# Kernel optimization log

Hardware: AMD Instinct MI355X
Metric: run time of the kernel (lower is better)

The kernel has to match this reference:

```python
import jax, jax.numpy as jnp
import numpy as np

nT, nB, H, V = 256, 256, 1024, 32000

def setup_inputs() -> dict:
    key = jax.random.key(0)
    ks = jax.random.split(key, 16)
    s = 0.02
    return {
        "tokens": jax.random.randint(ks[0], (nB,), 0, V),
        "prev_hidden": jax.random.normal(ks[1], (1, nB, H), dtype=jnp.float32),
        "enc_outputs": jax.random.normal(ks[2], (nT, nB, H), dtype=jnp.float32),
        "emb": jax.random.normal(ks[3], (V, H), dtype=jnp.float32) * s,
        "W_i2h": jax.random.normal(ks[4], (H, H), dtype=jnp.float32) * s,
        "W_h2h": jax.random.normal(ks[5], (H, H), dtype=jnp.float32) * s,
        "b_h2h": jnp.zeros((H,), dtype=jnp.float32),
        "w_score": jax.random.normal(ks[6], (H,), dtype=jnp.float32) * s,
        "W_ih": jax.random.normal(ks[7], (3 * H, 2 * H), dtype=jnp.float32) * s,
        "b_ih": jnp.zeros((3 * H,), dtype=jnp.float32),
        "W_hh": jax.random.normal(ks[8], (3 * H, H), dtype=jnp.float32) * s,
        "b_hh": jnp.zeros((3 * H,), dtype=jnp.float32),
        "W_out": jax.random.normal(ks[9], (V, H), dtype=jnp.float32) * s,
        "b_out": jnp.zeros((V,), dtype=jnp.float32),
    }

def reference(tokens, prev_hidden, enc_outputs, emb, W_i2h, W_h2h, b_h2h,
              w_score, W_ih, b_ih, W_hh, b_hh, W_out, b_out):
    h0 = prev_hidden[0]                                     # [nB,H]
    cur_emb = emb[tokens]                                   # [nB,H] (dropout = identity at inference)
    # additive (Bahdanau) attention energies
    enc_proj = jnp.einsum('tbh,oh->tbo', enc_outputs, W_i2h)  # [nT,nB,H]
    h_proj = h0 @ W_h2h.T + b_h2h                           # [nB,H]
    e = jnp.einsum('tbh,h->tb', jnp.tanh(enc_proj + h_proj[None]), w_score)  # [nT,nB]
    alpha = jax.nn.softmax(e.T, axis=1)                     # [nB,nT], softmax over time
    context = jnp.einsum('bt,tbh->bh', alpha, enc_outputs)  # [nB,H]
    x = jnp.concatenate([context, cur_emb], axis=1)         # [nB,2H]
    # single GRU step (PyTorch gate order: r, z, n)
    gi = x @ W_ih.T + b_ih                                  # [nB,3H]
    gh = h0 @ W_hh.T + b_hh                                 # [nB,3H]
    hs = h0.shape[-1]
    r = jax.nn.sigmoid(gi[:, :hs] + gh[:, :hs])
    z = jax.nn.sigmoid(gi[:, hs:2*hs] + gh[:, hs:2*hs])
    n = jnp.tanh(gi[:, 2*hs:] + r * gh[:, 2*hs:])
    h_new = (1.0 - z) * n + z * h0                          # [nB,H]
    out = jax.nn.log_softmax(h_new @ W_out.T + b_out, axis=1)  # [nB,V]
    return out, h_new[None], alpha
```

## Files before the change

kernel.cpp:

```cpp
#include <hip/hip_runtime.h>
#include <hip/hip_bf16.h>

typedef __attribute__((ext_vector_type(8))) short bf16x8;
typedef __attribute__((ext_vector_type(4))) float f32x4;
typedef __attribute__((ext_vector_type(4))) int i32x4;
typedef __attribute__((ext_vector_type(4))) unsigned short u16x4;
typedef __attribute__((ext_vector_type(8))) unsigned short u16x8;

#define LDS_STRIDE 72

__device__ __forceinline__ unsigned short f2bf(float f) {
    __hip_bfloat16 h = __float2bfloat16(f);
    unsigned short u; __builtin_memcpy(&u, &h, 2); return u;
}
__device__ __forceinline__ float bf2f(unsigned short u) {
    union { unsigned u; float f; } v; v.u = ((unsigned)u) << 16; return v.f;
}
__device__ __forceinline__ float fast_sigmoid(float x) { return 1.f / (1.f + __expf(-x)); }
__device__ __forceinline__ float fast_tanh(float x)    { return 1.f - 2.f / (__expf(2.f * x) + 1.f); }

#define GLOAD_LDS16(gp, lp) __builtin_amdgcn_global_load_lds( \
    (const __attribute__((address_space(1))) void*)(gp), \
    (__attribute__((address_space(3))) void*)(lp), 16, 0, 0)


#define STA(LB, HF, PTR) do { \
    GLOAD_LDS16((PTR), &AL[LB][HF][ldsrow][0]); \
    GLOAD_LDS16((PTR) + 65536, &AL[LB][HF][64 + ldsrow][0]); \
} while (0)

#define STB(LB, HF, PTR) do { \
    GLOAD_LDS16((PTR), &BL[LB][HF][ldsrow][0]); \
    GLOAD_LDS16((PTR) + 65536, &BL[LB][HF][64 + ldsrow][0]); \
} while (0)

#define LDA(DST, BUF, MH, KS) do { \
    const int c_ = ((KS)*32 + fg*8) ^ swzr; \
    _Pragma("unroll") \
    for (int mi = 0; mi < 4; ++mi) \
        DST[mi] = *(const bf16x8*)&AL[BUF][wr][(MH)*64 + mi*16 + fr][c_]; \
} while (0)

#define LDB(DST, BUF, KS) do { \
    const int c_ = ((KS)*32 + fg*8) ^ swzr; \
    _Pragma("unroll") \
    for (int ni = 0; ni < 4; ++ni) \
        DST[ni] = *(const bf16x8*)&BL[BUF][bh][br0 + ni*16 + fr][c_]; \
} while (0)

#define MM(AV, BV, MH) do { \
    _Pragma("unroll") \
    for (int mi = 0; mi < 4; ++mi) \
        _Pragma("unroll") \
        for (int ni = 0; ni < 4; ++ni) \
            acc[(MH)*4 + mi][ni] = __builtin_amdgcn_mfma_f32_16x16x32_bf16( \
                AV[mi], BV[ni], acc[(MH)*4 + mi][ni], 0, 0, 0); \
} while (0)

#define SP1 __builtin_amdgcn_s_setprio(1)
#define SP0 __builtin_amdgcn_s_setprio(0)
#define BAR asm volatile("s_barrier" ::: "memory")
#define VMC4 asm volatile("s_waitcnt vmcnt(4)" ::: "memory")
#define VMC0 asm volatile("s_waitcnt vmcnt(0)" ::: "memory")

__global__ __launch_bounds__(512, 1)
void gemm8p_e(const unsigned short* __restrict__ Ag, const unsigned short* __restrict__ Bg,
              const float* __restrict__ hproj, const float* __restrict__ wscore,
              float* __restrict__ epart)
{
    const int tid = threadIdx.x;
    const int lane = tid & 63, wid = tid >> 6;
    const int fr = lane & 15, fg = lane >> 4;
    const int wr = wid >> 2;
    const int wc = wid & 3;
    const int bh = wc >> 1, br0 = (wc & 1) * 64;

    const int cpx = (int)gridDim.x >> 3;
    const int swz = ((int)blockIdx.x & 7) * cpx + ((int)blockIdx.x >> 3);
    const int mb = swz >> 2, nb = swz & 3;
    const int m0 = mb << 8, n0 = nb << 8;

    __shared__ unsigned short AL[2][2][128][64];
    __shared__ unsigned short BL[2][2][128][64];

    const int srow = lane >> 3;
    const int scol = ((lane & 7) ^ srow) << 3;
    const int swzr = (fr & 7) << 3;
    const int ldsrow = wid * 8;

    const unsigned short* pA0 = Ag + (size_t)(m0 + ldsrow + srow) * 1024 + scol;
    const unsigned short* pA1 = pA0 + (size_t)128 * 1024;
    const unsigned short* pB0 = Bg + (size_t)(n0 + ldsrow + srow) * 1024 + scol;
    const unsigned short* pB1 = pB0 + (size_t)128 * 1024;

    f32x4 acc[8][4];
#pragma unroll
    for (int i = 0; i < 8; ++i)
#pragma unroll
        for (int j = 0; j < 4; ++j) acc[i][j] = (f32x4){0.f, 0.f, 0.f, 0.f};
    bf16x8 avA[4], avB[4], bvA[4], bvB[4];

    STA(0, 0, pA0); STA(0, 1, pA1);
    STB(0, 0, pB0); STB(0, 1, pB1);
    STB(1, 0, pB0 + 64); STB(1, 1, pB1 + 64);
    VMC4;
    BAR;

#pragma unroll
    for (int t = 0; t < 16; t += 2) {
        const int tof = t * 64;
        LDB(bvA, 0, 0); LDA(avA, 0, 0, 0);
        SP1; MM(avA, bvA, 0); SP0;
        LDB(bvB, 0, 1); LDA(avB, 0, 0, 1);
        if (t + 1 < 16) STA(1, 0, pA0 + tof + 64);
        BAR;
        SP1; MM(avB, bvB, 0); SP0;
        LDA(avA, 0, 1, 0);
        if (t + 1 < 16) STA(1, 1, pA1 + tof + 64);
        BAR;
        SP1; MM(avA, bvA, 1); SP0;
        LDA(avB, 0, 1, 1);
        if (t + 2 < 16) STB(0, 0, pB0 + tof + 128);
        BAR;
        SP1; MM(avB, bvB, 1); SP0;
        if (t + 2 < 16) { STB(0, 1, pB1 + tof + 128); VMC4; } else { VMC0; }
        BAR;
        LDB(bvA, 1, 0); LDA(avA, 1, 0, 0);
        SP1; MM(avA, bvA, 0); SP0;
        LDB(bvB, 1, 1); LDA(avB, 1, 0, 1);
        if (t + 2 < 16) STA(0, 0, pA0 + tof + 128);
        BAR;
        SP1; MM(avB, bvB, 0); SP0;
        LDA(avA, 1, 1, 0);
        if (t + 2 < 16) STA(0, 1, pA1 + tof + 128);
        BAR;
        SP1; MM(avA, bvA, 1); SP0;
        LDA(avB, 1, 1, 1);
        if (t + 3 < 16) STB(1, 0, pB0 + tof + 192);
        BAR;
        SP1; MM(avB, bvB, 1); SP0;
        if (t + 3 < 16) { STB(1, 1, pB1 + tof + 192); VMC4; }
        BAR;
    }

    float wsv[4];
#pragma unroll
    for (int ni = 0; ni < 4; ++ni) wsv[ni] = wscore[n0 + wc * 64 + ni * 16 + fr];
#pragma unroll
    for (int mi = 0; mi < 8; ++mi)
#pragma unroll
        for (int r = 0; r < 4; ++r) {
            const int bb = wr * 128 + mi * 16 + fg * 4 + r;
            const float* hp = hproj + (size_t)bb * 1024 + n0 + wc * 64 + fr;
            float s = 0.f;
#pragma unroll
            for (int ni = 0; ni < 4; ++ni)
                s += fast_tanh(acc[mi][ni][r] + hp[ni * 16]) * wsv[ni];
            s += __shfl_xor(s, 1); s += __shfl_xor(s, 2);
            s += __shfl_xor(s, 4); s += __shfl_xor(s, 8);
            if (fr == 0) epart[((size_t)bb * 256 + mb) * 16 + nb * 4 + wc] = s;
        }
}

template<int EPI, bool ABF, bool BBF>
__global__ __launch_bounds__(256, 2)
void gemm_rs(const void* __restrict__ Agv, const void* __restrict__ Bgv,
             const float* __restrict__ bias, float* __restrict__ Cout,
             unsigned short* __restrict__ CoutB,
             const float* __restrict__ hproj, const float* __restrict__ wscore,
             float* __restrict__ epart, float* __restrict__ lsepart,
             int M, int N, int K)
{
    const int nbn = N >> 7;
    const int nmb = M >> 7;
    int mb, nb;
    if (EPI == 1) {
        int cpx = gridDim.x >> 3;
        int bp = (blockIdx.x & 7) * cpx + (blockIdx.x >> 3);
        mb = bp / nbn; nb = bp % nbn;
    } else {
        mb = blockIdx.x % nmb; nb = blockIdx.x / nmb;
    }
    const int m0 = mb << 7, n0 = nb << 7;
    const int tid = threadIdx.x;
    const int lane = tid & 63, wid = tid >> 6;
    const int fr = lane & 15, fg = lane >> 4;
    const int srow = tid >> 1, shalf = (tid & 1) * 32;

    extern __shared__ char smem[];
    typedef unsigned short (*tile_t)[128][LDS_STRIDE];
    tile_t As = (tile_t)smem;
    tile_t Bs = (tile_t)(smem + 2 * 128 * LDS_STRIDE * 2);

    const float* Af = (const float*)Agv;
    const unsigned short* Ab = (const unsigned short*)Agv;
    const float* Bf = (const float*)Bgv;
    const unsigned short* Bb = (const unsigned short*)Bgv;

    f32x4 acc[2][8];
#pragma unroll
    for (int i = 0; i < 2; ++i)
#pragma unroll
        for (int j = 0; j < 8; ++j) acc[i][j] = (f32x4){0.f, 0.f, 0.f, 0.f};

    float a_f[32]; unsigned short a_b[32];
    float b_f[32]; unsigned short b_b[32];

    auto loadA = [&](int kt) {
        size_t base = (size_t)(m0 + srow) * K + (size_t)kt * 64 + shalf;
        if (ABF) {
#pragma unroll
            for (int j = 0; j < 4; ++j) *(i32x4*)&a_b[j * 8] = *(const i32x4*)(Ab + base + j * 8);
        } else {
#pragma unroll
            for (int j = 0; j < 8; ++j) *(f32x4*)&a_f[j * 4] = *(const f32x4*)(Af + base + j * 4);
        }
    };
    auto loadB = [&](int kt) {
        size_t base = (size_t)(n0 + srow) * K + (size_t)kt * 64 + shalf;
        if (BBF) {
#pragma unroll
            for (int j = 0; j < 4; ++j) *(i32x4*)&b_b[j * 8] = *(const i32x4*)(Bb + base + j * 8);
        } else {
#pragma unroll
            for (int j = 0; j < 8; ++j) *(f32x4*)&b_f[j * 4] = *(const f32x4*)(Bf + base + j * 4);
        }
    };
    auto storeA = [&](int buf) {
        unsigned short tA[32];
        if (ABF) {
#pragma unroll
            for (int j = 0; j < 32; ++j) tA[j] = a_b[j];
        } else {
#pragma unroll
            for (int j = 0; j < 32; ++j) tA[j] = f2bf(a_f[j]);
        }
#pragma unroll
        for (int j = 0; j < 4; ++j) *(i32x4*)&As[buf][srow][shalf + j * 8] = *(i32x4*)&tA[j * 8];
    };
    auto storeB = [&](int buf) {
        unsigned short tB[32];
        if (BBF) {
#pragma unroll
            for (int j = 0; j < 32; ++j) tB[j] = b_b[j];
        } else {
#pragma unroll
            for (int j = 0; j < 32; ++j) tB[j] = f2bf(b_f[j]);
        }
#pragma unroll
        for (int j = 0; j < 4; ++j) *(i32x4*)&Bs[buf][srow][shalf + j * 8] = *(i32x4*)&tB[j * 8];
    };

    const int nkt = K >> 6;

    loadA(0); loadB(0);
    storeA(0); storeB(0);
    __syncthreads();

    for (int kt = 0; kt < nkt; ++kt) {
        const int cur = kt & 1;
        if (kt + 1 < nkt) { loadA(kt + 1); loadB(kt + 1); }
#pragma unroll
        for (int ks = 0; ks < 2; ++ks) {
            bf16x8 av[2], bv[8];
#pragma unroll
            for (int mi = 0; mi < 2; ++mi)
                av[mi] = *(const bf16x8*)&As[cur][wid * 32 + mi * 16 + fr][ks * 32 + fg * 8];
#pragma unroll
            for (int ni = 0; ni < 8; ++ni)
                bv[ni] = *(const bf16x8*)&Bs[cur][ni * 16 + fr][ks * 32 + fg * 8];
#pragma unroll
            for (int mi = 0; mi < 2; ++mi)
#pragma unroll
                for (int ni = 0; ni < 8; ++ni)
                    acc[mi][ni] = __builtin_amdgcn_mfma_f32_16x16x32_bf16(av[mi], bv[ni], acc[mi][ni], 0, 0, 0);
        }
        if (kt + 1 < nkt) { storeA(cur ^ 1); storeB(cur ^ 1); }
        __syncthreads();
    }

    if (EPI == 0) {
#pragma unroll
        for (int mi = 0; mi < 2; ++mi)
#pragma unroll
            for (int r = 0; r < 4; ++r) {
                const int m = m0 + wid * 32 + mi * 16 + fg * 4 + r;
#pragma unroll
                for (int ni = 0; ni < 8; ++ni) {
                    const int col = n0 + ni * 16 + fr;
                    Cout[(size_t)m * N + col] = acc[mi][ni][r] + bias[col];
                }
            }
    } else if (EPI == 1) {
        float wsv[8];
#pragma unroll
        for (int ni = 0; ni < 8; ++ni) wsv[ni] = wscore[n0 + ni * 16 + fr];
#pragma unroll
        for (int mi = 0; mi < 2; ++mi)
#pragma unroll
            for (int r = 0; r < 4; ++r) {
                const int m = m0 + wid * 32 + mi * 16 + fg * 4 + r;
                const int bb = m & 255, tt = m >> 8;
                const float* hp = hproj + (size_t)bb * 1024 + n0 + fr;
                float s = 0.f;
#pragma unroll
                for (int ni = 0; ni < 8; ++ni)
                    s += fast_tanh(acc[mi][ni][r] + hp[ni * 16]) * wsv[ni];
                s += __shfl_xor(s, 1); s += __shfl_xor(s, 2);
                s += __shfl_xor(s, 4); s += __shfl_xor(s, 8);
                if (fr == 0) epart[((size_t)bb * 256 + tt) * 8 + nb] = s;
            }
    } else {
#pragma unroll
        for (int mi = 0; mi < 2; ++mi)
#pragma unroll
            for (int r = 0; r < 4; ++r) {
                const int m = m0 + wid * 32 + mi * 16 + fg * 4 + r;
                float vv[8];
                float mx = -3.4e38f;
#pragma unroll
                for (int ni = 0; ni < 8; ++ni) {
                    const int col = n0 + ni * 16 + fr;
                    vv[ni] = acc[mi][ni][r] + bias[col];
                    CoutB[(size_t)m * N + col] = f2bf(vv[ni]);
                    mx = fmaxf(mx, vv[ni]);
                }
                mx = fmaxf(mx, __shfl_xor(mx, 1));
                mx = fmaxf(mx, __shfl_xor(mx, 2));
                mx = fmaxf(mx, __shfl_xor(mx, 4));
                mx = fmaxf(mx, __shfl_xor(mx, 8));
                float se = 0.f;
#pragma unroll
                for (int ni = 0; ni < 8; ++ni) se += __expf(vv[ni] - mx);
                se += __shfl_xor(se, 1); se += __shfl_xor(se, 2);
                se += __shfl_xor(se, 4); se += __shfl_xor(se, 8);
                if (fr == 0) {
                    lsepart[((size_t)m * nbn + nb) * 2]     = mx;
                    lsepart[((size_t)m * nbn + nb) * 2 + 1] = se;
                }
            }
    }
}

__global__ void prep_all(const float* __restrict__ enc, unsigned short* __restrict__ encB,
                         const float* __restrict__ Wi2h, unsigned short* __restrict__ WiB,
                         const float* __restrict__ emb, const int* __restrict__ tokens,
                         unsigned short* __restrict__ xB)
{
    const int ENC4 = 16777216, WI4 = 262144, EMB4 = 65536;
    const int total = ENC4 + WI4 + EMB4;
    for (int i = blockIdx.x * 256 + threadIdx.x; i < total; i += gridDim.x * 256) {
        f32x4 v; unsigned short* dst;
        if (i < ENC4) {
            v = *(const f32x4*)(enc + (size_t)i * 4);
            dst = encB + (size_t)i * 4;
        } else if (i < ENC4 + WI4) {
            int j = i - ENC4;
            v = *(const f32x4*)(Wi2h + (size_t)j * 4);
            dst = WiB + (size_t)j * 4;
        } else {
            int j = i - ENC4 - WI4;
            int b = j >> 8, h4 = j & 255;
            v = *(const f32x4*)(emb + (size_t)tokens[b] * 1024 + h4 * 4);
            dst = xB + (size_t)b * 2048 + 1024 + h4 * 4;
        }
        u16x4 o;
#pragma unroll
        for (int j = 0; j < 4; ++j) o[j] = f2bf(v[j]);
        *(u16x4*)dst = o;
    }
}

__global__ void prep_kernel(const float* __restrict__ Wi2h, unsigned short* __restrict__ WiB,
                            const float* __restrict__ emb, const int* __restrict__ tokens,
                            unsigned short* __restrict__ xB)
{
    int i = blockIdx.x * 256 + threadIdx.x;
    if (i < 262144) {
        f32x4 v = *(const f32x4*)(Wi2h + (size_t)i * 4);
        u16x4 o;
#pragma unroll
        for (int j = 0; j < 4; ++j) o[j] = f2bf(v[j]);
        *(u16x4*)(WiB + (size_t)i * 4) = o;
    } else {
        int j = i - 262144;
        int b = j >> 8, h4 = j & 255;
        int tok = tokens[b];
        f32x4 v = *(const f32x4*)(emb + (size_t)tok * 1024 + h4 * 4);
        u16x4 o;
#pragma unroll
        for (int jj = 0; jj < 4; ++jj) o[jj] = f2bf(v[jj]);
        *(u16x4*)(xB + (size_t)b * 2048 + 1024 + h4 * 4) = o;
    }
}

__global__ __launch_bounds__(256) void softmax_alpha(const float* __restrict__ epart,
                                                     float* __restrict__ alpha, int pw)
{
    const int b = blockIdx.x, t = threadIdx.x;
    const int lane = t & 63, w = t >> 6;
    const float* ep = epart + ((size_t)b * 256 + t) * pw;
    float s = 0.f;
    for (int j = 0; j < pw; ++j) s += ep[j];
    __shared__ float rmax[4], rsum[4];
    float mx = s;
#pragma unroll
    for (int d = 1; d < 64; d <<= 1) mx = fmaxf(mx, __shfl_xor(mx, d));
    if (lane == 0) rmax[w] = mx;
    __syncthreads();
    mx = fmaxf(fmaxf(rmax[0], rmax[1]), fmaxf(rmax[2], rmax[3]));
    float p = __expf(s - mx);
    float sm = p;
#pragma unroll
    for (int d = 1; d < 64; d <<= 1) sm += __shfl_xor(sm, d);
    if (lane == 0) rsum[w] = sm;
    __syncthreads();
    sm = rsum[0] + rsum[1] + rsum[2] + rsum[3];
    alpha[(size_t)b * 256 + t] = p / sm;
}

__global__ __launch_bounds__(128) void ctx_part_bf(const float* __restrict__ alpha,
                                                   const unsigned short* __restrict__ encB,
                                                   float* __restrict__ pc)
{
    const int b = blockIdx.x, tc = blockIdx.y;
    const int h8 = threadIdx.x;
    const float* al = alpha + (size_t)b * 256 + tc * 64;
    float acc[8];
#pragma unroll
    for (int j = 0; j < 8; ++j) acc[j] = 0.f;
#pragma unroll 4
    for (int i = 0; i < 64; ++i) {
        float a = al[i];
        u16x8 e = *(const u16x8*)(encB + ((size_t)(tc * 64 + i) * 256 + b) * 1024 + h8 * 8);
#pragma unroll
        for (int j = 0; j < 8; ++j) acc[j] += bf2f(e[j]) * a;
    }
    float* d = pc + ((size_t)tc * 256 + b) * 1024 + h8 * 8;
    *(f32x4*)d = *(f32x4*)&acc[0];
    *(f32x4*)(d + 4) = *(f32x4*)&acc[4];
}

__global__ __launch_bounds__(256) void ctx_part(const float* __restrict__ alpha,
                                                const float* __restrict__ enc,
                                                float* __restrict__ pc)
{
    const int b = blockIdx.x, tc = blockIdx.y;
    const int h4 = threadIdx.x;
    const float* al = alpha + (size_t)b * 256 + tc * 64;
    f32x4 acc = {0.f, 0.f, 0.f, 0.f};
#pragma unroll 4
    for (int i = 0; i < 64; ++i) {
        float a = al[i];
        f32x4 e = *(const f32x4*)(enc + ((size_t)(tc * 64 + i) * 256 + b) * 1024 + h4 * 4);
        acc += e * a;
    }
    *(f32x4*)(pc + ((size_t)tc * 256 + b) * 1024 + h4 * 4) = acc;
}

__global__ void ctx_fin(const float* __restrict__ pc, unsigned short* __restrict__ xB)
{
    const int b = blockIdx.x, h4 = threadIdx.x;
    f32x4 c = {0.f, 0.f, 0.f, 0.f};
#pragma unroll
    for (int tc = 0; tc < 4; ++tc)
        c += *(const f32x4*)(pc + ((size_t)tc * 256 + b) * 1024 + h4 * 4);
    u16x4 o;
#pragma unroll
    for (int j = 0; j < 4; ++j) o[j] = f2bf(c[j]);
    *(u16x4*)(xB + (size_t)b * 2048 + h4 * 4) = o;
}

__global__ void gru_kernel(const float* __restrict__ gi, const float* __restrict__ gh,
                           const float* __restrict__ h0, float* __restrict__ hnew,
                           unsigned short* __restrict__ hnB)
{
    int idx = blockIdx.x * 256 + threadIdx.x;
    int b = idx >> 10, h = idx & 1023;
    size_t gb = (size_t)b * 3072;
    float r = fast_sigmoid(gi[gb + h]        + gh[gb + h]);
    float z = fast_sigmoid(gi[gb + 1024 + h] + gh[gb + 1024 + h]);
    float n = fast_tanh   (gi[gb + 2048 + h] + r * gh[gb + 2048 + h]);
    float hp = h0[idx];
    float hn = (1.f - z) * n + z * hp;
    hnew[idx] = hn;
    hnB[idx] = f2bf(hn);
}

__global__ void lse_reduce(const float* __restrict__ lsepart, float* __restrict__ lse, int nbn)
{
    const int m = blockIdx.x, l = threadIdx.x;
    float mx = -3.4e38f, s = 0.f;
    for (int p = l; p < nbn; p += 64) {
        float pm = lsepart[((size_t)m * nbn + p) * 2];
        float ps = lsepart[((size_t)m * nbn + p) * 2 + 1];
        float nm = fmaxf(mx, pm);
        s = s * __expf(mx - nm) + ps * __expf(pm - nm);
        mx = nm;
    }
#pragma unroll
    for (int d = 1; d < 64; d <<= 1) {
        float om = __shfl_xor(mx, d), os = __shfl_xor(s, d);
        float nm = fmaxf(mx, om);
        s = s * __expf(mx - nm) + os * __expf(om - nm);
        mx = nm;
    }
    if (l == 0) lse[m] = mx + __logf(s);
}

__global__ void lsub_bf(const unsigned short* __restrict__ lgB,
                        const float* __restrict__ lse, float* __restrict__ out)
{
    int f = blockIdx.x * 256 + threadIdx.x;
    float l = lse[f / 4000];
    u16x8 v = *(const u16x8*)(lgB + (size_t)f * 8);
    float* o = out + (size_t)f * 8;
    f32x4 o0, o1;
#pragma unroll
    for (int j = 0; j < 4; ++j) o0[j] = bf2f(v[j]) - l;
#pragma unroll
    for (int j = 0; j < 4; ++j) o1[j] = bf2f(v[4 + j]) - l;
    *(f32x4*)o = o0;
    *(f32x4*)(o + 4) = o1;
}

extern "C" void kernel_launch(void* const* d_in, const int* in_sizes, int n_in,
                              void* d_out, int out_size, void* d_ws, size_t ws_size,
                              hipStream_t stream)
{
    const int*   tokens  = (const int*)  d_in[0];
    const float* h0      = (const float*)d_in[1];
    const float* enc     = (const float*)d_in[2];
    const float* emb     = (const float*)d_in[3];
    const float* W_i2h   = (const float*)d_in[4];
    const float* W_h2h   = (const float*)d_in[5];
    const float* b_h2h   = (const float*)d_in[6];
    const float* w_score = (const float*)d_in[7];
    const float* W_ih    = (const float*)d_in[8];
    const float* b_ih    = (const float*)d_in[9];
    const float* W_hh    = (const float*)d_in[10];
    const float* b_hh    = (const float*)d_in[11];
    const float* W_out   = (const float*)d_in[12];
    const float* b_out   = (const float*)d_in[13];

    float* out   = (float*)d_out;
    float* hnew  = out + (size_t)256 * 32000;
    float* alpha = hnew + 256 * 1024;

    const size_t RS_LDS = 2u * 2u * 128u * LDS_STRIDE * 2u;

    char* w = (char*)d_ws;
    const size_t NEED = (size_t)153 * (1 << 20);

    if (ws_size >= NEED) {
        unsigned short* encB  = (unsigned short*)(w);
        unsigned short* lgB   = (unsigned short*)(w);
        unsigned short* WiB   = (unsigned short*)(w + (size_t)128 * (1 << 20));
        float* hproj          = (float*)(w + (size_t)130 * (1 << 20));
        float* gh             = (float*)(w + (size_t)131 * (1 << 20));
        float* epart          = (float*)(w + (size_t)134 * (1 << 20));
        float* pc             = (float*)(w + (size_t)138 * (1 << 20));
        unsigned short* xB    = (unsigned short*)(w + (size_t)142 * (1 << 20));
        float* gi             = (float*)(w + (size_t)143 * (1 << 20));
        unsigned short* hnB   = (unsigned short*)(w + (size_t)146 * (1 << 20));
        float* lsepart        = (float*)(w + (size_t)147 * (1 << 20));
        float* lse            = (float*)(w + (size_t)148 * (1 << 20));

        prep_all<<<2048, 256, 0, stream>>>(enc, encB, W_i2h, WiB, emb, tokens, xB);
        gemm_rs<0, false, false><<<16, 256, RS_LDS, stream>>>(h0, W_h2h, b_h2h, hproj,
            nullptr, nullptr, nullptr, nullptr, nullptr, 256, 1024, 1024);
        gemm_rs<0, false, false><<<48, 256, RS_LDS, stream>>>(h0, W_hh, b_hh, gh,
            nullptr, nullptr, nullptr, nullptr, nullptr, 256, 3072, 1024);
        gemm8p_e<<<1024, 512, 0, stream>>>(encB, WiB, hproj, w_score, epart);
        softmax_alpha<<<256, 256, 0, stream>>>(epart, alpha, 16);
        ctx_part_bf<<<dim3(256, 4), 128, 0, stream>>>(alpha, encB, pc);
        ctx_fin<<<256, 256, 0, stream>>>(pc, xB);
        gemm_rs<0, true, false><<<48, 256, RS_LDS, stream>>>(xB, W_ih, b_ih, gi,
            nullptr, nullptr, nullptr, nullptr, nullptr, 256, 3072, 2048);
        gru_kernel<<<1024, 256, 0, stream>>>(gi, gh, h0, hnew, hnB);
        gemm_rs<2, true, false><<<500, 256, RS_LDS, stream>>>(hnB, W_out, b_out, nullptr,
            lgB, nullptr, nullptr, nullptr, lsepart, 256, 32000, 1024);
        lse_reduce<<<256, 64, 0, stream>>>(lsepart, lse, 250);
        lsub_bf<<<4000, 256, 0, stream>>>(lgB, lse, out);
    } else {
        unsigned short* WiB   = (unsigned short*)(w);
        float* hproj          = (float*)(w + (size_t)2  * (1 << 20));
        float* gh             = (float*)(w + (size_t)3  * (1 << 20));
        float* epart          = (float*)(w + (size_t)6  * (1 << 20));
        float* pc             = (float*)(w + (size_t)8  * (1 << 20));
        unsigned short* xB    = (unsigned short*)(w + (size_t)12 * (1 << 20));
        float* gi             = (float*)(w + (size_t)13 * (1 << 20));
        unsigned short* hnB   = (unsigned short*)(w + (size_t)16 * (1 << 20));
        float* lsepart        = (float*)(w + (size_t)17 * (1 << 20));
        float* lse            = (float*)(w + (size_t)18 * (1 << 20));
        unsigned short* lgB   = (unsigned short*)(w + (size_t)19 * (1 << 20));

        prep_kernel<<<1280, 256, 0, stream>>>(W_i2h, WiB, emb, tokens, xB);
        gemm_rs<0, false, false><<<16, 256, RS_LDS, stream>>>(h0, W_h2h, b_h2h, hproj,
            nullptr, nullptr, nullptr, nullptr, nullptr, 256, 1024, 1024);
        gemm_rs<0, false, false><<<48, 256, RS_LDS, stream>>>(h0, W_hh, b_hh, gh,
            nullptr, nullptr, nullptr, nullptr, nullptr, 256, 3072, 1024);
        gemm_rs<1, false, true><<<4096, 256, RS_LDS, stream>>>(enc, WiB, nullptr, nullptr,
            nullptr, hproj, w_score, epart, nullptr, 65536, 1024, 1024);
        softmax_alpha<<<256, 256, 0, stream>>>(epart, alpha, 8);
        ctx_part<<<dim3(256, 4), 256, 0, stream>>>(alpha, enc, pc);
        ctx_fin<<<256, 256, 0, stream>>>(pc, xB);
        gemm_rs<0, true, false><<<48, 256, RS_LDS, stream>>>(xB, W_ih, b_ih, gi,
            nullptr, nullptr, nullptr, nullptr, nullptr, 256, 3072, 2048);
        gru_kernel<<<1024, 256, 0, stream>>>(gi, gh, h0, hnew, hnB);
        gemm_rs<2, true, false><<<500, 256, RS_LDS, stream>>>(hnB, W_out, b_out, nullptr,
            lgB, nullptr, nullptr, nullptr, lsepart, 256, 32000, 1024);
        lse_reduce<<<256, 64, 0, stream>>>(lsepart, lse, 250);
        lsub_bf<<<4000, 256, 0, stream>>>(lgB, lse, out);
    }
}
```

Baseline: 515.0 us.

## Triple-buffer A tiles in attention GEMM and merge two h0 GEMMs into one launch

The main attention-energy GEMM now keeps three LDS buffers for the A (encoder) tile instead of two. Loads are issued two k-steps ahead, and the wait counts are raised to vmcnt(8) so more global-to-LDS traffic stays in flight. Separately, the two small GEMMs on h0 (W_h2h and W_hh) are merged into one 64-block kernel to save a launch and fill more CUs. The extra LDS buffer raises shared memory use per block, and the deeper prefetch depends on correct rotation of the buffer indices.

After: 479.3 us. 1.07x faster.

```diff
diff --git a/kernel.cpp b/kernel.cpp
--- a/kernel.cpp
+++ b/kernel.cpp
@@ -60,7 +60,7 @@
 #define SP1 __builtin_amdgcn_s_setprio(1)
 #define SP0 __builtin_amdgcn_s_setprio(0)
 #define BAR asm volatile("s_barrier" ::: "memory")
-#define VMC4 asm volatile("s_waitcnt vmcnt(4)" ::: "memory")
+#define VMC8 asm volatile("s_waitcnt vmcnt(8)" ::: "memory")
 #define VMC0 asm volatile("s_waitcnt vmcnt(0)" ::: "memory")
 
 __global__ __launch_bounds__(512, 1)
@@ -80,7 +80,7 @@
     const int mb = swz >> 2, nb = swz & 3;
     const int m0 = mb << 8, n0 = nb << 8;
 
-    __shared__ unsigned short AL[2][2][128][64];
+    __shared__ unsigned short AL[3][2][128][64];
     __shared__ unsigned short BL[2][2][128][64];
 
     const int srow = lane >> 3;
@@ -100,46 +100,48 @@
         for (int j = 0; j < 4; ++j) acc[i][j] = (f32x4){0.f, 0.f, 0.f, 0.f};
     bf16x8 avA[4], avB[4], bvA[4], bvB[4];
 
-    STA(0, 0, pA0); STA(0, 1, pA1);
-    STB(0, 0, pB0); STB(0, 1, pB1);
+    STA(0, 0, pA0);      STA(0, 1, pA1);
+    STB(0, 0, pB0);      STB(0, 1, pB1);
+    STA(1, 0, pA0 + 64); STA(1, 1, pA1 + 64);
     STB(1, 0, pB0 + 64); STB(1, 1, pB1 + 64);
-    VMC4;
+    VMC8;
     BAR;
 
 #pragma unroll
     for (int t = 0; t < 16; t += 2) {
         const int tof = t * 64;
-        LDB(bvA, 0, 0); LDA(avA, 0, 0, 0);
+        const int a0 = t % 3, a1 = (t + 1) % 3, a2 = (t + 2) % 3, a3 = (t + 3) % 3;
+        LDB(bvA, 0, 0); LDA(avA, a0, 0, 0);
         SP1; MM(avA, bvA, 0); SP0;
-        LDB(bvB, 0, 1); LDA(avB, 0, 0, 1);
-        if (t + 1 < 16) STA(1, 0, pA0 + tof + 64);
+        LDB(bvB, 0, 1); LDA(avB, a0, 0, 1);
+        if (t + 2 < 16) STA(a2, 0, pA0 + tof + 128);
         BAR;
         SP1; MM(avB, bvB, 0); SP0;
-        LDA(avA, 0, 1, 0);
-        if (t + 1 < 16) STA(1, 1, pA1 + tof + 64);
+        LDA(avA, a0, 1, 0);
+        if (t + 2 < 16) STA(a2, 1, pA1 + tof + 128);
         BAR;
         SP1; MM(avA, bvA, 1); SP0;
-        LDA(avB, 0, 1, 1);
+        LDA(avB, a0, 1, 1);
         if (t + 2 < 16) STB(0, 0, pB0 + tof + 128);
         BAR;
         SP1; MM(avB, bvB, 1); SP0;
-        if (t + 2 < 16) { STB(0, 1, pB1 + tof + 128); VMC4; } else { VMC0; }
+        if (t + 2 < 16) { STB(0, 1, pB1 + tof + 128); VMC8; } else { VMC0; }
         BAR;
-        LDB(bvA, 1, 0); LDA(avA, 1, 0, 0);
+        LDB(bvA, 1, 0); LDA(avA, a1, 0, 0);
         SP1; MM(avA, bvA, 0); SP0;
-        LDB(bvB, 1, 1); LDA(avB, 1, 0, 1);
-        if (t + 2 < 16) STA(0, 0, pA0 + tof + 128);
+        LDB(bvB, 1, 1); LDA(avB, a1, 0, 1);
+        if (t + 3 < 16) STA(a3, 0, pA0 + tof + 192);
         BAR;
         SP1; MM(avB, bvB, 0); SP0;
-        LDA(avA, 1, 1, 0);
-        if (t + 2 < 16) STA(0, 1, pA1 + tof + 128);
+        LDA(avA, a1, 1, 0);
+        if (t + 3 < 16) STA(a3, 1, pA1 + tof + 192);
         BAR;
         SP1; MM(avA, bvA, 1); SP0;
-        LDA(avB, 1, 1, 1);
+        LDA(avB, a1, 1, 1);
         if (t + 3 < 16) STB(1, 0, pB0 + tof + 192);
         BAR;
         SP1; MM(avB, bvB, 1); SP0;
-        if (t + 3 < 16) { STB(1, 1, pB1 + tof + 192); VMC4; }
+        if (t + 3 < 16) { STB(1, 1, pB1 + tof + 192); VMC8; }
         BAR;
     }
 
@@ -159,6 +161,101 @@
             s += __shfl_xor(s, 1); s += __shfl_xor(s, 2);
             s += __shfl_xor(s, 4); s += __shfl_xor(s, 8);
             if (fr == 0) epart[((size_t)bb * 256 + mb) * 16 + nb * 4 + wc] = s;
+        }
+}
+
+__global__ __launch_bounds__(256, 2)
+void gemm_h2(const float* __restrict__ h0,
+             const float* __restrict__ Wh2h, const float* __restrict__ Whh,
+             const float* __restrict__ bh2h, const float* __restrict__ bhh,
+             float* __restrict__ hproj, float* __restrict__ gh)
+{
+    const int mb = blockIdx.x & 1;
+    const int nbg = blockIdx.x >> 1;
+    const float* Bf; const float* bias; float* Cout; int Nst; int n0;
+    if (nbg < 8) { Bf = Wh2h; bias = bh2h; Cout = hproj; Nst = 1024; n0 = nbg << 7; }
+    else         { Bf = Whh;  bias = bhh;  Cout = gh;    Nst = 3072; n0 = (nbg - 8) << 7; }
+
+    const int m0 = mb << 7;
+    const int tid = threadIdx.x;
+    const int lane = tid & 63, wid = tid >> 6;
+    const int fr = lane & 15, fg = lane >> 4;
+    const int srow = tid >> 1, shalf = (tid & 1) * 32;
+
+    extern __shared__ char smem[];
+    typedef unsigned short (*tile_t)[128][LDS_STRIDE];
+    tile_t As = (tile_t)smem;
+    tile_t Bs = (tile_t)(smem + 2 * 128 * LDS_STRIDE * 2);
+
+    f32x4 acc[2][8];
+#pragma unroll
+    for (int i = 0; i < 2; ++i)
+#pragma unroll
+        for (int j = 0; j < 8; ++j) acc[i][j] = (f32x4){0.f, 0.f, 0.f, 0.f};
+
+    float a_f[32], b_f[32];
+
+    auto loadA = [&](int kt) {
+        size_t base = (size_t)(m0 + srow) * 1024 + (size_t)kt * 64 + shalf;
+#pragma unroll
+        for (int j = 0; j < 8; ++j) *(f32x4*)&a_f[j * 4] = *(const f32x4*)(h0 + base + j * 4);
+    };
+    auto loadB = [&](int kt) {
+        size_t base = (size_t)(n0 + srow) * 1024 + (size_t)kt * 64 + shalf;
+#pragma unroll
+        for (int j = 0; j < 8; ++j) *(f32x4*)&b_f[j * 4] = *(const f32x4*)(Bf + base + j * 4);
+    };
+    auto storeA = [&](int buf) {
+        unsigned short t[32];
+#pragma unroll
+        for (int j = 0; j < 32; ++j) t[j] = f2bf(a_f[j]);
+#pragma unroll
+        for (int j = 0; j < 4; ++j) *(i32x4*)&As[buf][srow][shalf + j * 8] = *(i32x4*)&t[j * 8];
+    };
+    auto storeB = [&](int buf) {
+        unsigned short t[32];
+#pragma unroll
+        for (int j = 0; j < 32; ++j) t[j] = f2bf(b_f[j]);
+#pragma unroll
+        for (int j = 0; j < 4; ++j) *(i32x4*)&Bs[buf][srow][shalf + j * 8] = *(i32x4*)&t[j * 8];
+    };
+
+    loadA(0); loadB(0);
+    storeA(0); storeB(0);
+    __syncthreads();
+
+    for (int kt = 0; kt < 16; ++kt) {
+        const int cur = kt & 1;
+        if (kt + 1 < 16) { loadA(kt + 1); loadB(kt + 1); }
+#pragma unroll
+        for (int ks = 0; ks < 2; ++ks) {
+            bf16x8 av[2], bv[8];
+#pragma unroll
+            for (int mi = 0; mi < 2; ++mi)
+                av[mi] = *(const bf16x8*)&As[cur][wid * 32 + mi * 16 + fr][ks * 32 + fg * 8];
+#pragma unroll
+            for (int ni = 0; ni < 8; ++ni)
+                bv[ni] = *(const bf16x8*)&Bs[cur][ni * 16 + fr][ks * 32 + fg * 8];
+#pragma unroll
+            for (int mi = 0; mi < 2; ++mi)
+#pragma unroll
+                for (int ni = 0; ni < 8; ++ni)
+                    acc[mi][ni] = __builtin_amdgcn_mfma_f32_16x16x32_bf16(av[mi], bv[ni], acc[mi][ni], 0, 0, 0);
+        }
+        if (kt + 1 < 16) { storeA(cur ^ 1); storeB(cur ^ 1); }
+        __syncthreads();
+    }
+
+#pragma unroll
+    for (int mi = 0; mi < 2; ++mi)
+#pragma unroll
+        for (int r = 0; r < 4; ++r) {
+            const int m = m0 + wid * 32 + mi * 16 + fg * 4 + r;
+#pragma unroll
+            for (int ni = 0; ni < 8; ++ni) {
+                const int col = n0 + ni * 16 + fr;
+                Cout[(size_t)m * Nst + col] = acc[mi][ni][r] + bias[col];
+            }
         }
 }
 
@@ -567,10 +664,7 @@
         float* lse            = (float*)(w + (size_t)148 * (1 << 20));
 
         prep_all<<<2048, 256, 0, stream>>>(enc, encB, W_i2h, WiB, emb, tokens, xB);
-        gemm_rs<0, false, false><<<16, 256, RS_LDS, stream>>>(h0, W_h2h, b_h2h, hproj,
-            nullptr, nullptr, nullptr, nullptr, nullptr, 256, 1024, 1024);
-        gemm_rs<0, false, false><<<48, 256, RS_LDS, stream>>>(h0, W_hh, b_hh, gh,
-            nullptr, nullptr, nullptr, nullptr, nullptr, 256, 3072, 1024);
+        gemm_h2<<<64, 256, RS_LDS, stream>>>(h0, W_h2h, W_hh, b_h2h, b_hh, hproj, gh);
         gemm8p_e<<<1024, 512, 0, stream>>>(encB, WiB, hproj, w_score, epart);
         softmax_alpha<<<256, 256, 0, stream>>>(epart, alpha, 16);
         ctx_part_bf<<<dim3(256, 4), 128, 0, stream>>>(alpha, encB, pc);
@@ -596,10 +690,7 @@
         unsigned short* lgB   = (unsigned short*)(w + (size_t)19 * (1 << 20));
 
         prep_kernel<<<1280, 256, 0, stream>>>(W_i2h, WiB, emb, tokens, xB);
-        gemm_rs<0, false, false><<<16, 256, RS_LDS, stream>>>(h0, W_h2h, b_h2h, hproj,
-            nullptr, nullptr, nullptr, nullptr, nullptr, 256, 1024, 1024);
-        gemm_rs<0, false, false><<<48, 256, RS_LDS, stream>>>(h0, W_hh, b_hh, gh,
-            nullptr, nullptr, nullptr, nullptr, nullptr, 256, 3072, 1024);
+        gemm_h2<<<64, 256, RS_LDS, stream>>>(h0, W_h2h, W_hh, b_h2h, b_hh, hproj, gh);
         gemm_rs<1, false, true><<<4096, 256, RS_LDS, stream>>>(enc, WiB, nullptr, nullptr,
             nullptr, hproj, w_score, epart, nullptr, 65536, 1024, 1024);
         softmax_alpha<<<256, 256, 0, stream>>>(epart, alpha, 8);
```
